# Performance work log

Hardware: AMD Instinct MI355X
Metric: run time of the kernel (lower is better)

## Reference

```python
import jax, jax.numpy as jnp
import numpy as np

N = 65536   # nodes
E = 262144  # edges
IN = 16     # input node feat dim
H0 = 16     # layer0 out dim
H1 = 8      # layer1 out dim (H0 // 2)
EA = 10     # edge attr dim (hardcoded in edge_nn)


def setup_inputs() -> dict:
    key = jax.random.key(0)
    ks = jax.random.split(key, 12)
    s = 0.05
    return {
        "x": jax.random.normal(ks[0], (N, IN), jnp.float32),
        "edge_index": jax.random.randint(ks[1], (2, E), 0, N),
        "edge_attr": jax.random.normal(ks[2], (E, EA), jnp.float32),
        # layer 0 edge MLP: Linear(10, 256) -> ReLU -> Linear(256, IN*H0)
        "w1_0": jax.random.normal(ks[3], (EA, H0 * H0), jnp.float32) * s,
        "b1_0": jnp.zeros((H0 * H0,), jnp.float32),
        "w2_0": jax.random.normal(ks[4], (H0 * H0, IN * H0), jnp.float32) * s,
        "b2_0": jnp.zeros((IN * H0,), jnp.float32),
        "root_0": jax.random.normal(ks[5], (IN, H0), jnp.float32) * s,
        "bias_0": jnp.zeros((H0,), jnp.float32),
        # layer 1 edge MLP: Linear(10, 256) -> ReLU -> Linear(256, H0*H1)
        "w1_1": jax.random.normal(ks[6], (EA, H0 * H0), jnp.float32) * s,
        "b1_1": jnp.zeros((H0 * H0,), jnp.float32),
        "w2_1": jax.random.normal(ks[7], (H0 * H0, H0 * H1), jnp.float32) * s,
        "b2_1": jnp.zeros((H0 * H1,), jnp.float32),
        "root_1": jax.random.normal(ks[8], (H0, H1), jnp.float32) * s,
        "bias_1": jnp.zeros((H1,), jnp.float32),
        # final edge classifier fc: Linear(2*H1, 1)
        "fc_w": jax.random.normal(ks[9], (2 * H1, 1), jnp.float32) * s,
        "fc_b": jnp.zeros((1,), jnp.float32),
    }


def _nnconv(x, src, dst, edge_attr, w1, b1, w2, b2, root, bias, in_c, out_c):
    # edge-conditioned weight generation: MLP(edge_attr) -> [E, in_c, out_c]
    h = jax.nn.relu(edge_attr @ w1 + b1)                 # [E, hid]
    We = (h @ w2 + b2).reshape(-1, in_c, out_c)          # [E, in, out]
    msg = jnp.einsum('ei,eio->eo', x[src], We)           # per-edge matmul [E, out]
    ssum = jax.ops.segment_sum(msg, dst, num_segments=N)               # [N, out]
    cnt = jax.ops.segment_sum(jnp.ones((msg.shape[0],), msg.dtype), dst, num_segments=N)
    agg = ssum / jnp.maximum(cnt, 1.0)[:, None]          # scatter-mean
    return agg + x @ root + bias                         # root transform + bias


def reference(x, edge_index, edge_attr, w1_0, b1_0, w2_0, b2_0, root_0, bias_0,
              w1_1, b1_1, w2_1, b2_1, root_1, bias_1, fc_w, fc_b):
    src, dst = edge_index[0], edge_index[1]
    # dropout is identity in eval mode
    x = jax.nn.relu(_nnconv(x, src, dst, edge_attr, w1_0, b1_0, w2_0, b2_0, root_0, bias_0, IN, H0))
    x = jax.nn.relu(_nnconv(x, src, dst, edge_attr, w1_1, b1_1, w2_1, b2_1, root_1, bias_1, H0, H1))
    ef = jnp.concatenate([x[src], x[dst]], axis=-1)      # [E, 2*H1]
    return jax.nn.sigmoid(ef @ fc_w + fc_b)              # [E, 1]
```

## Files before the change

kernel.cpp:

```cpp
#include <hip/hip_runtime.h>
#include <stdint.h>

#define NN 65536
#define NE 262144

typedef __attribute__((ext_vector_type(8))) short bf16x8;
typedef __attribute__((ext_vector_type(4))) float f32x4;

__device__ __forceinline__ short f2bf(float f) {
  union { float f; uint32_t u; } v; v.f = f;
  uint32_t u = v.u + 0x7fffu + ((v.u >> 16) & 1u);
  return (short)(u >> 16);
}
__device__ __forceinline__ uint32_t pack2(float a, float b) {
  return (uint32_t)(uint16_t)f2bf(a) | ((uint32_t)(uint16_t)f2bf(b) << 16);
}

__global__ __launch_bounds__(256) void prep_all(
    const float* __restrict__ ea, short* __restrict__ eab,
    const float* __restrict__ w1_0, const float* __restrict__ w1_1,
    const float* __restrict__ w2_0, const float* __restrict__ w2_1,
    short* __restrict__ w1t0, short* __restrict__ w1t1,
    short* __restrict__ w2t0, short* __restrict__ w2t1) {
  int idx = blockIdx.x * 256 + threadIdx.x;
  {
    int e = idx >> 4, k = idx & 15;
    eab[idx] = (k < 10) ? f2bf(ea[e * 10 + k]) : (short)0;
  }
  if (idx < 65536) {
    if (idx < 8192) {
      int n = idx >> 5, k = idx & 31;
      w1t0[idx] = (k < 10) ? f2bf(w1_0[k * 256 + n]) : (short)0;
      w1t1[idx] = (k < 10) ? f2bf(w1_1[k * 256 + n]) : (short)0;
    }
    if (idx < 32768) {
      int n = idx >> 8, k = idx & 255;
      w2t1[idx] = f2bf(w2_1[k * 128 + n]);
    }
    {
      int n = idx >> 8, k = idx & 255;
      w2t0[idx] = f2bf(w2_0[k * 256 + n]);
    }
  }
}

template <int N2, int OUTC, bool DO_CNT>
__global__ __launch_bounds__(256) void edge_kernel(
    const float* __restrict__ x, const int* __restrict__ ei,
    const short* __restrict__ eab, const short* __restrict__ w1t,
    const float* __restrict__ b1, const short* __restrict__ w2t,
    const float* __restrict__ b2, float* __restrict__ ssum,
    float* __restrict__ cnt) {
  constexpr int NT2 = N2 / 64;
  constexpr int LOGO = (OUTC == 16) ? 4 : 3;
  constexpr int SLOTS = 4 * (16 / OUTC);
  constexpr int PADO = OUTC + 1;
  __shared__ alignas(16) char smem[64 * 256 * 2 + 64 * 20 * 4];
  char* const hB = smem;
  float* const partial = (float*)smem;
  float* const xs = (float*)(smem + 64 * 256 * 2);

  const int tid = threadIdx.x;
  const int wave = tid >> 6;
  const int lane = tid & 63;
  const int g = lane >> 4;
  const int lr = lane & 15;
  const int e0 = blockIdx.x * 64;

  bf16x8 aw[4];
#pragma unroll
  for (int ml = 0; ml < 4; ++ml)
    aw[ml] = *(const bf16x8*)(w1t + ((wave * 4 + ml) * 16 + lr) * 32 + g * 8);
  bf16x8 be[4];
#pragma unroll
  for (int et = 0; et < 4; ++et) {
    if (g < 2)
      be[et] = *(const bf16x8*)(eab + (size_t)(e0 + et * 16 + lr) * 16 + g * 8);
    else
      be[et] = (bf16x8){0, 0, 0, 0, 0, 0, 0, 0};
  }

  bf16x8 bcur[NT2];
#pragma unroll
  for (int nt = 0; nt < NT2; ++nt) {
    int colo = wave * (NT2 * 16) + nt * 16 + lr;
    bcur[nt] = *(const bf16x8*)(w2t + colo * 256 + g * 8);
  }

  {
    int e = tid >> 2, q = tid & 3;
    int s = ei[e0 + e];
    float4 v = *(const float4*)(x + (size_t)s * 16 + q * 4);
    *(float4*)(xs + e * 20 + q * 4) = v;
  }

  {
    f32x4 acc1[4][4];
#pragma unroll
    for (int ml = 0; ml < 4; ++ml)
#pragma unroll
      for (int et = 0; et < 4; ++et) acc1[ml][et] = (f32x4){0.f, 0.f, 0.f, 0.f};
#pragma unroll
    for (int et = 0; et < 4; ++et)
#pragma unroll
      for (int ml = 0; ml < 4; ++ml)
        acc1[ml][et] = __builtin_amdgcn_mfma_f32_16x16x32_bf16(aw[ml], be[et], acc1[ml][et], 0, 0, 0);
#pragma unroll
    for (int ml = 0; ml < 4; ++ml) {
      int kb = (wave * 4 + ml) * 16 + g * 4;
      float4 bb = *(const float4*)(b1 + kb);
#pragma unroll
      for (int et = 0; et < 4; ++et) {
        int e = et * 16 + lr;
        float v0 = fmaxf(acc1[ml][et][0] + bb.x, 0.f);
        float v1 = fmaxf(acc1[ml][et][1] + bb.y, 0.f);
        float v2 = fmaxf(acc1[ml][et][2] + bb.z, 0.f);
        float v3 = fmaxf(acc1[ml][et][3] + bb.w, 0.f);
        int2 w; w.x = (int)pack2(v0, v1); w.y = (int)pack2(v2, v3);
        *(int2*)(hB + ((e * 512 + kb * 2) ^ ((e & 7) << 4))) = w;
      }
    }
  }
  __syncthreads();

  f32x4 acc[4][NT2];
#pragma unroll
  for (int mt = 0; mt < 4; ++mt)
#pragma unroll
    for (int nt = 0; nt < NT2; ++nt) acc[mt][nt] = (f32x4){0.f, 0.f, 0.f, 0.f};
#pragma unroll
  for (int ks = 0; ks < 8; ++ks) {
    bf16x8 bnxt[NT2];
    if (ks < 7) {
#pragma unroll
      for (int nt = 0; nt < NT2; ++nt) {
        int colo = wave * (NT2 * 16) + nt * 16 + lr;
        bnxt[nt] = *(const bf16x8*)(w2t + colo * 256 + (ks + 1) * 32 + g * 8);
      }
    }
    bf16x8 a2[4];
#pragma unroll
    for (int mt = 0; mt < 4; ++mt) {
      int e = mt * 16 + lr;
      a2[mt] = *(const bf16x8*)(hB + ((e * 512 + ks * 64 + g * 16) ^ ((e & 7) << 4)));
    }
#pragma unroll
    for (int nt = 0; nt < NT2; ++nt)
#pragma unroll
      for (int mt = 0; mt < 4; ++mt)
        acc[mt][nt] = __builtin_amdgcn_mfma_f32_16x16x32_bf16(a2[mt], bcur[nt], acc[mt][nt], 0, 0, 0);
    if (ks < 7) {
#pragma unroll
      for (int nt = 0; nt < NT2; ++nt) bcur[nt] = bnxt[nt];
    }
  }
  __syncthreads();

  const int o = lr & (OUTC - 1);
  const int slot = wave * (16 / OUTC) + (lr >> LOGO);
  float b2c[NT2];
  int iv[NT2];
#pragma unroll
  for (int nt = 0; nt < NT2; ++nt) {
    int colo = wave * (NT2 * 16) + nt * 16 + lr;
    b2c[nt] = b2[colo];
    iv[nt] = colo >> LOGO;
  }
#pragma unroll
  for (int mt = 0; mt < 4; ++mt)
#pragma unroll
    for (int r = 0; r < 4; ++r) {
      int e = mt * 16 + g * 4 + r;
      float m = 0.f;
#pragma unroll
      for (int nt = 0; nt < NT2; ++nt)
        m += (acc[mt][nt][r] + b2c[nt]) * xs[e * 20 + iv[nt]];
      partial[(slot * 64 + e) * PADO + o] = m;
    }
  __syncthreads();

  constexpr int REP = 64 * OUTC / 256;
  {
    int e = tid >> 2;
    int d = ei[NE + e0 + e];
#pragma unroll
    for (int j = 0; j < REP; ++j) {
      int pr = tid * REP + j;
      int oo = pr & (OUTC - 1);
      float s = 0.f;
#pragma unroll
      for (int sl = 0; sl < SLOTS; ++sl) s += partial[(sl * 64 + e) * PADO + oo];
      atomicAdd(&ssum[(size_t)d * OUTC + oo], s);
    }
  }
  if (DO_CNT && tid < 64) atomicAdd(&cnt[ei[NE + e0 + tid]], 1.0f);
}

template <int OUTC>
__global__ __launch_bounds__(256) void node_kernel(
    const float* __restrict__ xin, const float* __restrict__ ssum,
    const float* __restrict__ cnt, const float* __restrict__ root,
    const float* __restrict__ bias, float* __restrict__ xout) {
  int n = blockIdx.x * 256 + threadIdx.x;
  float inv = 1.0f / fmaxf(cnt[n], 1.0f);
  float xi[16];
#pragma unroll
  for (int i = 0; i < 4; ++i) {
    float4 v = ((const float4*)(xin + (size_t)n * 16))[i];
    xi[4 * i] = v.x; xi[4 * i + 1] = v.y; xi[4 * i + 2] = v.z; xi[4 * i + 3] = v.w;
  }
#pragma unroll
  for (int o = 0; o < OUTC; ++o) {
    float a = ssum[(size_t)n * OUTC + o] * inv + bias[o];
#pragma unroll
    for (int i = 0; i < 16; ++i) a += xi[i] * root[i * OUTC + o];
    xout[(size_t)n * OUTC + o] = fmaxf(a, 0.f);
  }
}

__global__ __launch_bounds__(256) void final_kernel(
    const float* __restrict__ x2, const int* __restrict__ ei,
    const float* __restrict__ fcw, const float* __restrict__ fcb,
    float* __restrict__ out) {
  int e = blockIdx.x * 256 + threadIdx.x;
  int s = ei[e], d = ei[NE + e];
  float acc = fcb[0];
  const float* xsr = x2 + (size_t)s * 8;
  const float* xdr = x2 + (size_t)d * 8;
#pragma unroll
  for (int c = 0; c < 8; ++c) acc += xsr[c] * fcw[c];
#pragma unroll
  for (int c = 0; c < 8; ++c) acc += xdr[c] * fcw[8 + c];
  out[e] = 1.0f / (1.0f + __expf(-acc));
}

extern "C" void kernel_launch(void* const* d_in, const int* in_sizes, int n_in,
                              void* d_out, int out_size, void* d_ws, size_t ws_size,
                              hipStream_t stream) {
  const float* x      = (const float*)d_in[0];
  const int*   ei     = (const int*)d_in[1];
  const float* ea     = (const float*)d_in[2];
  const float* w1_0   = (const float*)d_in[3];
  const float* b1_0   = (const float*)d_in[4];
  const float* w2_0   = (const float*)d_in[5];
  const float* b2_0   = (const float*)d_in[6];
  const float* root_0 = (const float*)d_in[7];
  const float* bias_0 = (const float*)d_in[8];
  const float* w1_1   = (const float*)d_in[9];
  const float* b1_1   = (const float*)d_in[10];
  const float* w2_1   = (const float*)d_in[11];
  const float* b2_1   = (const float*)d_in[12];
  const float* root_1 = (const float*)d_in[13];
  const float* bias_1 = (const float*)d_in[14];
  const float* fc_w   = (const float*)d_in[15];
  const float* fc_b   = (const float*)d_in[16];
  float* out = (float*)d_out;

  char* ws = (char*)d_ws;
  float* ssum0 = (float*)(ws);
  float* x1    = (float*)(ws + (4u << 20));
  float* ssum1 = (float*)(ws + (8u << 20));
  float* x2    = (float*)(ws + (10u << 20));
  float* cnt   = (float*)(ws + (12u << 20));
  short* w1t0  = (short*)(ws + (12u << 20) + (256u << 10));
  short* w1t1  = w1t0 + 8192;
  short* w2t0  = w1t1 + 8192;
  short* w2t1  = w2t0 + 65536;
  short* eab   = w2t1 + 32768;

  hipMemsetAsync(ssum0, 0, (size_t)NN * 16 * 4, stream);
  hipMemsetAsync(ssum1, 0, (size_t)NN * 8 * 4, stream);
  hipMemsetAsync(cnt, 0, (size_t)NN * 4, stream);
  prep_all<<<NE * 16 / 256, 256, 0, stream>>>(ea, eab, w1_0, w1_1, w2_0, w2_1,
                                              w1t0, w1t1, w2t0, w2t1);

  edge_kernel<256, 16, true><<<NE / 64, 256, 0, stream>>>(
      x, ei, eab, w1t0, b1_0, w2t0, b2_0, ssum0, cnt);
  node_kernel<16><<<NN / 256, 256, 0, stream>>>(x, ssum0, cnt, root_0, bias_0, x1);
  edge_kernel<128, 8, false><<<NE / 64, 256, 0, stream>>>(
      x1, ei, eab, w1t1, b1_1, w2t1, b2_1, ssum1, nullptr);
  node_kernel<8><<<NN / 256, 256, 0, stream>>>(x1, ssum1, cnt, root_1, bias_1, x2);
  final_kernel<<<NE / 256, 256, 0, stream>>>(x2, ei, fc_w, fc_b, out);
}
```

Before: 190.4 us.

## Process 128 edges per 512-thread block in edge kernel with hardware bf16 pack

Each edge-kernel block now handles 128 edges with 8 waves instead of 64 edges with 4. Each wave covers a narrower column slice of the second MLP GEMM and all 8 edge tiles, so every w2 fragment loaded is reused across twice as many edges. The cross-wave partial reduction is restructured, and the OUTC=8 layer adds a shuffle to fold the two half-columns. The software float-to-bf16 rounding is replaced by the v_cvt_pk_bf16_f32 instruction. Shared memory per block grows to about 74KB and the 8x NT2 accumulator array raises register pressure, which may limit occupancy.

```diff
diff --git a/kernel.cpp b/kernel.cpp
--- a/kernel.cpp
+++ b/kernel.cpp
@@ -12,8 +12,10 @@
   uint32_t u = v.u + 0x7fffu + ((v.u >> 16) & 1u);
   return (short)(u >> 16);
 }
-__device__ __forceinline__ uint32_t pack2(float a, float b) {
-  return (uint32_t)(uint16_t)f2bf(a) | ((uint32_t)(uint16_t)f2bf(b) << 16);
+__device__ __forceinline__ uint32_t cvtpk(float lo, float hi) {
+  uint32_t r;
+  asm("v_cvt_pk_bf16_f32 %0, %1, %2" : "=v"(r) : "v"(lo), "v"(hi));
+  return r;
 }
 
 __global__ __launch_bounds__(256) void prep_all(
@@ -45,87 +47,90 @@
 }
 
 template <int N2, int OUTC, bool DO_CNT>
-__global__ __launch_bounds__(256) void edge_kernel(
+__global__ __launch_bounds__(512, 4) void edge_kernel(
     const float* __restrict__ x, const int* __restrict__ ei,
     const short* __restrict__ eab, const short* __restrict__ w1t,
     const float* __restrict__ b1, const short* __restrict__ w2t,
     const float* __restrict__ b2, float* __restrict__ ssum,
     float* __restrict__ cnt) {
-  constexpr int NT2 = N2 / 64;
+  constexpr int WCOLS = N2 / 8;
+  constexpr int NT2 = WCOLS / 16;
   constexpr int LOGO = (OUTC == 16) ? 4 : 3;
-  constexpr int SLOTS = 4 * (16 / OUTC);
   constexpr int PADO = OUTC + 1;
-  __shared__ alignas(16) char smem[64 * 256 * 2 + 64 * 20 * 4];
+  constexpr int PARTSZ = 8 * 128 * PADO * 4;
+  constexpr int XSOFF = (PARTSZ > 65536) ? PARTSZ : 65536;
+  __shared__ alignas(16) char smem[XSOFF + 128 * 20 * 4];
   char* const hB = smem;
   float* const partial = (float*)smem;
-  float* const xs = (float*)(smem + 64 * 256 * 2);
+  float* const xs = (float*)(smem + XSOFF);
 
   const int tid = threadIdx.x;
-  const int wave = tid >> 6;
+  const int w = tid >> 6;
   const int lane = tid & 63;
   const int g = lane >> 4;
   const int lr = lane & 15;
-  const int e0 = blockIdx.x * 64;
-
-  bf16x8 aw[4];
-#pragma unroll
-  for (int ml = 0; ml < 4; ++ml)
-    aw[ml] = *(const bf16x8*)(w1t + ((wave * 4 + ml) * 16 + lr) * 32 + g * 8);
-  bf16x8 be[4];
-#pragma unroll
-  for (int et = 0; et < 4; ++et) {
+  const int e0 = blockIdx.x * 128;
+
+  const int eR = tid >> 2;
+  const int qR = tid & 3;
+  const int dR = ei[NE + e0 + eR];
+  {
+    int s = ei[e0 + eR];
+    float4 v = *(const float4*)(x + (size_t)s * 16 + qR * 4);
+    *(float4*)(xs + eR * 20 + qR * 4) = v;
+  }
+
+  bf16x8 aw[2];
+#pragma unroll
+  for (int ml = 0; ml < 2; ++ml)
+    aw[ml] = *(const bf16x8*)(w1t + ((w * 2 + ml) * 16 + lr) * 32 + g * 8);
+  bf16x8 be[8];
+#pragma unroll
+  for (int et = 0; et < 8; ++et) {
     if (g < 2)
       be[et] = *(const bf16x8*)(eab + (size_t)(e0 + et * 16 + lr) * 16 + g * 8);
     else
       be[et] = (bf16x8){0, 0, 0, 0, 0, 0, 0, 0};
   }
 
+  f32x4 acc1[2][8];
+#pragma unroll
+  for (int ml = 0; ml < 2; ++ml)
+#pragma unroll
+    for (int et = 0; et < 8; ++et) acc1[ml][et] = (f32x4){0.f, 0.f, 0.f, 0.f};
+#pragma unroll
+  for (int et = 0; et < 8; ++et)
+#pragma unroll
+    for (int ml = 0; ml < 2; ++ml)
+      acc1[ml][et] = __builtin_amdgcn_mfma_f32_16x16x32_bf16(aw[ml], be[et], acc1[ml][et], 0, 0, 0);
+
   bf16x8 bcur[NT2];
 #pragma unroll
   for (int nt = 0; nt < NT2; ++nt) {
-    int colo = wave * (NT2 * 16) + nt * 16 + lr;
+    int colo = w * WCOLS + nt * 16 + lr;
     bcur[nt] = *(const bf16x8*)(w2t + colo * 256 + g * 8);
   }
 
-  {
-    int e = tid >> 2, q = tid & 3;
-    int s = ei[e0 + e];
-    float4 v = *(const float4*)(x + (size_t)s * 16 + q * 4);
-    *(float4*)(xs + e * 20 + q * 4) = v;
-  }
-
-  {
-    f32x4 acc1[4][4];
-#pragma unroll
-    for (int ml = 0; ml < 4; ++ml)
-#pragma unroll
-      for (int et = 0; et < 4; ++et) acc1[ml][et] = (f32x4){0.f, 0.f, 0.f, 0.f};
-#pragma unroll
-    for (int et = 0; et < 4; ++et)
-#pragma unroll
-      for (int ml = 0; ml < 4; ++ml)
-        acc1[ml][et] = __builtin_amdgcn_mfma_f32_16x16x32_bf16(aw[ml], be[et], acc1[ml][et], 0, 0, 0);
-#pragma unroll
-    for (int ml = 0; ml < 4; ++ml) {
-      int kb = (wave * 4 + ml) * 16 + g * 4;
-      float4 bb = *(const float4*)(b1 + kb);
-#pragma unroll
-      for (int et = 0; et < 4; ++et) {
-        int e = et * 16 + lr;
-        float v0 = fmaxf(acc1[ml][et][0] + bb.x, 0.f);
-        float v1 = fmaxf(acc1[ml][et][1] + bb.y, 0.f);
-        float v2 = fmaxf(acc1[ml][et][2] + bb.z, 0.f);
-        float v3 = fmaxf(acc1[ml][et][3] + bb.w, 0.f);
-        int2 w; w.x = (int)pack2(v0, v1); w.y = (int)pack2(v2, v3);
-        *(int2*)(hB + ((e * 512 + kb * 2) ^ ((e & 7) << 4))) = w;
-      }
+#pragma unroll
+  for (int ml = 0; ml < 2; ++ml) {
+    int kb = (w * 2 + ml) * 16 + g * 4;
+    float4 bb = *(const float4*)(b1 + kb);
+#pragma unroll
+    for (int et = 0; et < 8; ++et) {
+      int e = et * 16 + lr;
+      float v0 = fmaxf(acc1[ml][et][0] + bb.x, 0.f);
+      float v1 = fmaxf(acc1[ml][et][1] + bb.y, 0.f);
+      float v2 = fmaxf(acc1[ml][et][2] + bb.z, 0.f);
+      float v3 = fmaxf(acc1[ml][et][3] + bb.w, 0.f);
+      int2 pw; pw.x = (int)cvtpk(v0, v1); pw.y = (int)cvtpk(v2, v3);
+      *(int2*)(hB + ((e * 512 + kb * 2) ^ ((e & 7) << 4))) = pw;
     }
   }
   __syncthreads();
 
-  f32x4 acc[4][NT2];
-#pragma unroll
-  for (int mt = 0; mt < 4; ++mt)
+  f32x4 acc[8][NT2];
+#pragma unroll
+  for (int mt = 0; mt < 8; ++mt)
 #pragma unroll
     for (int nt = 0; nt < NT2; ++nt) acc[mt][nt] = (f32x4){0.f, 0.f, 0.f, 0.f};
 #pragma unroll
@@ -134,21 +139,25 @@
     if (ks < 7) {
 #pragma unroll
       for (int nt = 0; nt < NT2; ++nt) {
-        int colo = wave * (NT2 * 16) + nt * 16 + lr;
+        int colo = w * WCOLS + nt * 16 + lr;
         bnxt[nt] = *(const bf16x8*)(w2t + colo * 256 + (ks + 1) * 32 + g * 8);
       }
     }
-    bf16x8 a2[4];
-#pragma unroll
-    for (int mt = 0; mt < 4; ++mt) {
-      int e = mt * 16 + lr;
-      a2[mt] = *(const bf16x8*)(hB + ((e * 512 + ks * 64 + g * 16) ^ ((e & 7) << 4)));
-    }
-#pragma unroll
-    for (int nt = 0; nt < NT2; ++nt)
-#pragma unroll
-      for (int mt = 0; mt < 4; ++mt)
-        acc[mt][nt] = __builtin_amdgcn_mfma_f32_16x16x32_bf16(a2[mt], bcur[nt], acc[mt][nt], 0, 0, 0);
+#pragma unroll
+    for (int hf = 0; hf < 2; ++hf) {
+      bf16x8 a2[4];
+#pragma unroll
+      for (int m4 = 0; m4 < 4; ++m4) {
+        int e = (hf * 4 + m4) * 16 + lr;
+        a2[m4] = *(const bf16x8*)(hB + ((e * 512 + ks * 64 + g * 16) ^ ((e & 7) << 4)));
+      }
+#pragma unroll
+      for (int nt = 0; nt < NT2; ++nt)
+#pragma unroll
+        for (int m4 = 0; m4 < 4; ++m4)
+          acc[hf * 4 + m4][nt] =
+              __builtin_amdgcn_mfma_f32_16x16x32_bf16(a2[m4], bcur[nt], acc[hf * 4 + m4][nt], 0, 0, 0);
+    }
     if (ks < 7) {
 #pragma unroll
       for (int nt = 0; nt < NT2; ++nt) bcur[nt] = bnxt[nt];
@@ -156,44 +165,42 @@
   }
   __syncthreads();
 
-  const int o = lr & (OUTC - 1);
-  const int slot = wave * (16 / OUTC) + (lr >> LOGO);
-  float b2c[NT2];
-  int iv[NT2];
-#pragma unroll
-  for (int nt = 0; nt < NT2; ++nt) {
-    int colo = wave * (NT2 * 16) + nt * 16 + lr;
-    b2c[nt] = b2[colo];
-    iv[nt] = colo >> LOGO;
-  }
-#pragma unroll
-  for (int mt = 0; mt < 4; ++mt)
-#pragma unroll
-    for (int r = 0; r < 4; ++r) {
-      int e = mt * 16 + g * 4 + r;
-      float m = 0.f;
-#pragma unroll
-      for (int nt = 0; nt < NT2; ++nt)
-        m += (acc[mt][nt][r] + b2c[nt]) * xs[e * 20 + iv[nt]];
-      partial[(slot * 64 + e) * PADO + o] = m;
-    }
+  {
+    const int o = lr & (OUTC - 1);
+    float b2c[NT2];
+    int iv[NT2];
+#pragma unroll
+    for (int nt = 0; nt < NT2; ++nt) {
+      int colo = w * WCOLS + nt * 16 + lr;
+      b2c[nt] = b2[colo];
+      iv[nt] = colo >> LOGO;
+    }
+#pragma unroll
+    for (int mt = 0; mt < 8; ++mt)
+#pragma unroll
+      for (int r = 0; r < 4; ++r) {
+        int e = mt * 16 + g * 4 + r;
+        float m = 0.f;
+#pragma unroll
+        for (int nt = 0; nt < NT2; ++nt)
+          m += (acc[mt][nt][r] + b2c[nt]) * xs[e * 20 + iv[nt]];
+        if (OUTC == 8) m += __shfl_xor(m, 8, 64);
+        partial[((size_t)w * 128 + e) * PADO + o] = m;
+      }
+  }
   __syncthreads();
 
-  constexpr int REP = 64 * OUTC / 256;
-  {
-    int e = tid >> 2;
-    int d = ei[NE + e0 + e];
-#pragma unroll
-    for (int j = 0; j < REP; ++j) {
-      int pr = tid * REP + j;
-      int oo = pr & (OUTC - 1);
+  if (qR * 4 < OUTC) {
+#pragma unroll
+    for (int j = 0; j < 4; ++j) {
+      int o = qR * 4 + j;
       float s = 0.f;
 #pragma unroll
-      for (int sl = 0; sl < SLOTS; ++sl) s += partial[(sl * 64 + e) * PADO + oo];
-      atomicAdd(&ssum[(size_t)d * OUTC + oo], s);
-    }
-  }
-  if (DO_CNT && tid < 64) atomicAdd(&cnt[ei[NE + e0 + tid]], 1.0f);
+      for (int sl = 0; sl < 8; ++sl) s += partial[((size_t)sl * 128 + eR) * PADO + o];
+      atomicAdd(&ssum[(size_t)dR * OUTC + o], s);
+    }
+  }
+  if (DO_CNT && tid < 128) atomicAdd(&cnt[ei[NE + e0 + tid]], 1.0f);
 }
 
 template <int OUTC>
@@ -274,10 +281,10 @@
   prep_all<<<NE * 16 / 256, 256, 0, stream>>>(ea, eab, w1_0, w1_1, w2_0, w2_1,
                                               w1t0, w1t1, w2t0, w2t1);
 
-  edge_kernel<256, 16, true><<<NE / 64, 256, 0, stream>>>(
+  edge_kernel<256, 16, true><<<NE / 128, 512, 0, stream>>>(
       x, ei, eab, w1t0, b1_0, w2t0, b2_0, ssum0, cnt);
   node_kernel<16><<<NN / 256, 256, 0, stream>>>(x, ssum0, cnt, root_0, bias_0, x1);
-  edge_kernel<128, 8, false><<<NE / 64, 256, 0, stream>>>(
+  edge_kernel<128, 8, false><<<NE / 128, 512, 0, stream>>>(
       x1, ei, eab, w1t1, b1_1, w2t1, b2_1, ssum1, nullptr);
   node_kernel<8><<<NN / 256, 256, 0, stream>>>(x1, ssum1, cnt, root_1, bias_1, x2);
   final_kernel<<<NE / 256, 256, 0, stream>>>(x2, ei, fc_w, fc_b, out);
```

New measurement: 215.7 us. 1.13x slower.
